# Kernel tuning notes

Hardware: AMD Instinct MI355X
Metric: run time of the kernel (lower is better)

## Reference

```python
import jax, jax.numpy as jnp
import numpy as np

SAMPLE_THRESH = 0.05  # self.sample_thresh


def grid_sample_bilinear_zeros(img, pts):
    """torch.nn.functional.grid_sample with mode='bilinear', align_corners=False,
    padding_mode='zeros'. img: [C, H, W]; pts: [N, 2] with (x, y) in [-1, 1].
    Returns [C, N]."""
    C, H, W = img.shape
    # align_corners=False unnormalization
    x = (pts[:, 0] + 1.0) * (W / 2.0) - 0.5
    y = (pts[:, 1] + 1.0) * (H / 2.0) - 0.5
    x0 = jnp.floor(x)
    y0 = jnp.floor(y)
    wx1 = x - x0
    wy1 = y - y0
    wx0 = 1.0 - wx1
    wy0 = 1.0 - wy1

    def gather(xi, yi):
        valid = (xi >= 0) & (xi < W) & (yi >= 0) & (yi < H)
        xi_c = jnp.clip(xi, 0, W - 1).astype(jnp.int32)
        yi_c = jnp.clip(yi, 0, H - 1).astype(jnp.int32)
        v = img[:, yi_c, xi_c]  # [C, N]
        return v * valid.astype(img.dtype)[None, :]

    out = (gather(x0, y0) * (wx0 * wy0)[None, :]
           + gather(x0 + 1, y0) * (wx1 * wy0)[None, :]
           + gather(x0, y0 + 1) * (wx0 * wy1)[None, :]
           + gather(x0 + 1, y0 + 1) * (wx1 * wy1)[None, :])
    return out


def setup_inputs() -> dict:
    key = jax.random.key(0)
    k1, k2, k3, k4 = jax.random.split(key, 4)
    N_A, N_B = 8192, 8192
    H, W2 = 504, 1008  # warp is [hs, 2*ws, 4] per post_process
    x_A = jax.random.uniform(k1, (N_A, 2), jnp.float32, -1.0, 1.0)
    x_B = jax.random.uniform(k2, (N_B, 2), jnp.float32, -1.0, 1.0)
    warp = jax.random.uniform(k3, (H, W2, 4), jnp.float32, -1.0, 1.0)
    certainty = jax.random.uniform(k4, (H, W2), jnp.float32, 0.0, 1.0)
    return {"x_A": x_A, "x_B": x_B, "warp": warp, "certainty": certainty}


def reference(x_A, x_B, warp, certainty):
    # --- match_keypoints ---
    # x_A_to_B = grid_sample(warp[..., -2:].permute(2,0,1)[None], x_A[None,None])[0,:,0].mT
    flow_img = jnp.transpose(warp[..., -2:], (2, 0, 1))  # [2, H, 2W]
    x_A_to_B = grid_sample_bilinear_zeros(flow_img, x_A).T  # [N_A, 2]
    cert_A_to_B = grid_sample_bilinear_zeros(certainty[None], x_A)[0]  # [N_A]

    # D = torch.cdist(x_A_to_B, x_B) via |a|^2 + |b|^2 - 2 a.b
    a2 = jnp.sum(x_A_to_B * x_A_to_B, axis=-1)  # [N_A]
    b2 = jnp.sum(x_B * x_B, axis=-1)            # [N_B]
    D2 = a2[:, None] + b2[None, :] - 2.0 * (x_A_to_B @ x_B.T)
    D = jnp.sqrt(jnp.maximum(D2, 1e-12))  # [N_A, N_B]

    # mutual nearest-neighbor mask with certainty threshold
    row_min = jnp.min(D, axis=-1, keepdims=True)
    col_min = jnp.min(D, axis=-2, keepdims=True)
    mask = (D == row_min) & (D == col_min) & (cert_A_to_B[:, None] > SAMPLE_THRESH)

    # jit-compatible equivalent of torch.nonzero: distances at mutual-NN pairs,
    # zero elsewhere. nonzero entries == matched (inds_A, inds_B) pairs.
    return jnp.where(mask, D, 0.0)
```

## Files before the change

kernel.cpp:

```cpp
#include <hip/hip_runtime.h>
#include <math.h>

#define SAMPLE_THRESH 0.05f

typedef float f32x4 __attribute__((ext_vector_type(4)));

__device__ __forceinline__ float d2_exact(float xa0, float xa1, float a2,
                                          float xb0, float xb1, float b2) {
    float p  = __fmul_rn(xa1, xb1);
    float q  = __fmaf_rn(xa0, xb0, p);
    float s  = __fadd_rn(a2, b2);
    return __fmaf_rn(-2.0f, q, s);
}

__device__ __forceinline__ float f_D(float d2) {
    return __fsqrt_rn(fmaxf(d2, 1e-12f));
}

__device__ __forceinline__ float nextf_pos(float x) {
    return __int_as_float(__float_as_int(x) + 1);
}
__device__ __forceinline__ float prevf_pos(float x) {
    return __int_as_float(__float_as_int(x) - 1);
}

__device__ __forceinline__ float hi_thresh(float m) {
    float t = f_D(m);
    float x = fmaxf(m, __fmul_rn(t, t));
    while (f_D(x) > t) x = prevf_pos(x);
    while (f_D(nextf_pos(x)) <= t) x = nextf_pos(x);
    return x;
}

__global__ __launch_bounds__(256) void sample_kernel(
    const float* __restrict__ xA, const float* __restrict__ xB,
    const float4* __restrict__ warp, const float* __restrict__ cert,
    float4* __restrict__ Apack, float4* __restrict__ Bpack,
    int nA, int nB, int H, int W) {
    int i = blockIdx.x * blockDim.x + threadIdx.x;
    if (i < nA) {
        float px = xA[2 * i + 0], py = xA[2 * i + 1];
        float xf = (px + 1.0f) * (0.5f * (float)W) - 0.5f;
        float yf = (py + 1.0f) * (0.5f * (float)H) - 0.5f;
        float x0f = floorf(xf), y0f = floorf(yf);
        float wx1 = xf - x0f, wy1 = yf - y0f;
        float wx0 = 1.0f - wx1, wy0 = 1.0f - wy1;
        int x0 = (int)x0f, y0 = (int)y0f;
        float fx = 0.0f, fy = 0.0f, cv = 0.0f;
#pragma unroll
        for (int dy = 0; dy < 2; ++dy) {
#pragma unroll
            for (int dx = 0; dx < 2; ++dx) {
                int xi = x0 + dx, yi = y0 + dy;
                float vm = (xi >= 0 && xi < W && yi >= 0 && yi < H) ? 1.0f : 0.0f;
                int xc = min(max(xi, 0), W - 1);
                int yc = min(max(yi, 0), H - 1);
                int idx = yc * W + xc;
                float4 wv = warp[idx];
                float  c  = cert[idx];
                float wgt = (dx ? wx1 : wx0) * (dy ? wy1 : wy0);
                fx += (wv.z * vm) * wgt;
                fy += (wv.w * vm) * wgt;
                cv += (c    * vm) * wgt;
            }
        }
        float a2 = fx * fx + fy * fy;
        Apack[i] = make_float4(fx, fy, a2, cv);
    }
    if (i < nB) {
        float b0 = xB[2 * i + 0], b1 = xB[2 * i + 1];
        Bpack[i] = make_float4(b0, b1, b0 * b0 + b1 * b1, 0.0f);
    }
}

__global__ __launch_bounds__(256) void min_kernel(
    const float4* __restrict__ Apack, const float4* __restrict__ Bpack,
    float4* __restrict__ rowpack, float* __restrict__ rowD,
    float4* __restrict__ colpack, int nA, int nB) {
    int gwave = (int)((blockIdx.x * blockDim.x + threadIdx.x) >> 6);
    int lane = threadIdx.x & 63;
    int nRowWaves = nA / 8;
    float m0 = 1e30f, m1 = 1e30f, m2 = 1e30f, m3 = 1e30f;
    float m4 = 1e30f, m5 = 1e30f, m6 = 1e30f, m7 = 1e30f;
    if (gwave < nRowWaves) {
        int i0 = gwave * 8;
        float4 A0 = Apack[i0 + 0], A1 = Apack[i0 + 1], A2 = Apack[i0 + 2], A3 = Apack[i0 + 3];
        float4 A4 = Apack[i0 + 4], A5 = Apack[i0 + 5], A6 = Apack[i0 + 6], A7 = Apack[i0 + 7];
        for (int j = lane; j < nB; j += 64) {
            float4 b = Bpack[j];
            m0 = fminf(m0, d2_exact(A0.x, A0.y, A0.z, b.x, b.y, b.z));
            m1 = fminf(m1, d2_exact(A1.x, A1.y, A1.z, b.x, b.y, b.z));
            m2 = fminf(m2, d2_exact(A2.x, A2.y, A2.z, b.x, b.y, b.z));
            m3 = fminf(m3, d2_exact(A3.x, A3.y, A3.z, b.x, b.y, b.z));
            m4 = fminf(m4, d2_exact(A4.x, A4.y, A4.z, b.x, b.y, b.z));
            m5 = fminf(m5, d2_exact(A5.x, A5.y, A5.z, b.x, b.y, b.z));
            m6 = fminf(m6, d2_exact(A6.x, A6.y, A6.z, b.x, b.y, b.z));
            m7 = fminf(m7, d2_exact(A7.x, A7.y, A7.z, b.x, b.y, b.z));
        }
#pragma unroll
        for (int o = 32; o; o >>= 1) {
            m0 = fminf(m0, __shfl_xor(m0, o, 64)); m1 = fminf(m1, __shfl_xor(m1, o, 64));
            m2 = fminf(m2, __shfl_xor(m2, o, 64)); m3 = fminf(m3, __shfl_xor(m3, o, 64));
            m4 = fminf(m4, __shfl_xor(m4, o, 64)); m5 = fminf(m5, __shfl_xor(m5, o, 64));
            m6 = fminf(m6, __shfl_xor(m6, o, 64)); m7 = fminf(m7, __shfl_xor(m7, o, 64));
        }
        if (lane == 0) {
#define ROW_OUT(K, AK, MK)                                                         \
            {                                                                      \
                float Dm = f_D(MK);                                                \
                float hi = (AK.w > SAMPLE_THRESH) ? hi_thresh(MK) : -1e30f;        \
                rowpack[i0 + K] = make_float4(AK.x, AK.y, AK.z, hi);               \
                rowD[i0 + K] = Dm;                                                 \
            }
            ROW_OUT(0, A0, m0) ROW_OUT(1, A1, m1) ROW_OUT(2, A2, m2) ROW_OUT(3, A3, m3)
            ROW_OUT(4, A4, m4) ROW_OUT(5, A5, m5) ROW_OUT(6, A6, m6) ROW_OUT(7, A7, m7)
#undef ROW_OUT
        }
    } else {
        int j0 = (gwave - nRowWaves) * 8;
        if (j0 >= nB) return;
        float4 B0 = Bpack[j0 + 0], B1 = Bpack[j0 + 1], B2 = Bpack[j0 + 2], B3 = Bpack[j0 + 3];
        float4 B4 = Bpack[j0 + 4], B5 = Bpack[j0 + 5], B6 = Bpack[j0 + 6], B7 = Bpack[j0 + 7];
        for (int i = lane; i < nA; i += 64) {
            float4 a = Apack[i];
            m0 = fminf(m0, d2_exact(a.x, a.y, a.z, B0.x, B0.y, B0.z));
            m1 = fminf(m1, d2_exact(a.x, a.y, a.z, B1.x, B1.y, B1.z));
            m2 = fminf(m2, d2_exact(a.x, a.y, a.z, B2.x, B2.y, B2.z));
            m3 = fminf(m3, d2_exact(a.x, a.y, a.z, B3.x, B3.y, B3.z));
            m4 = fminf(m4, d2_exact(a.x, a.y, a.z, B4.x, B4.y, B4.z));
            m5 = fminf(m5, d2_exact(a.x, a.y, a.z, B5.x, B5.y, B5.z));
            m6 = fminf(m6, d2_exact(a.x, a.y, a.z, B6.x, B6.y, B6.z));
            m7 = fminf(m7, d2_exact(a.x, a.y, a.z, B7.x, B7.y, B7.z));
        }
#pragma unroll
        for (int o = 32; o; o >>= 1) {
            m0 = fminf(m0, __shfl_xor(m0, o, 64)); m1 = fminf(m1, __shfl_xor(m1, o, 64));
            m2 = fminf(m2, __shfl_xor(m2, o, 64)); m3 = fminf(m3, __shfl_xor(m3, o, 64));
            m4 = fminf(m4, __shfl_xor(m4, o, 64)); m5 = fminf(m5, __shfl_xor(m5, o, 64));
            m6 = fminf(m6, __shfl_xor(m6, o, 64)); m7 = fminf(m7, __shfl_xor(m7, o, 64));
        }
        if (lane == 0) {
#define COL_OUT(K, BK, MK)                                                         \
            colpack[j0 + K] = make_float4(BK.x, BK.y, BK.z, hi_thresh(MK));
            COL_OUT(0, B0, m0) COL_OUT(1, B1, m1) COL_OUT(2, B2, m2) COL_OUT(3, B3, m3)
            COL_OUT(4, B4, m4) COL_OUT(5, B5, m5) COL_OUT(6, B6, m6) COL_OUT(7, B7, m7)
#undef COL_OUT
        }
    }
}

#define TI 64
#define TJ 1024
__global__ __launch_bounds__(256) void out_kernel(
    const float4* __restrict__ rowpack, const float* __restrict__ rowD,
    const float4* __restrict__ colpack, float* __restrict__ out, int N) {
    __shared__ float4 cp[TJ];
    __shared__ float4 rp[TI];
    __shared__ float rd[TI];
    int tid = threadIdx.x;
    int j0 = blockIdx.x * TJ;
    int i0 = blockIdx.y * TI;
    for (int k = tid; k < TJ; k += 256) cp[k] = colpack[j0 + k];
    if (tid < TI) { rp[tid] = rowpack[i0 + tid]; rd[tid] = rowD[i0 + tid]; }
    __syncthreads();
    float4 c0 = cp[tid * 4 + 0], c1 = cp[tid * 4 + 1];
    float4 c2 = cp[tid * 4 + 2], c3 = cp[tid * 4 + 3];
    size_t base = (size_t)i0 * (size_t)N + (size_t)j0 + (size_t)tid * 4;
#pragma unroll 2
    for (int r = 0; r < TI; ++r) {
        float4 a = rp[r];
        float Dm = rd[r];
        float d0 = d2_exact(a.x, a.y, a.z, c0.x, c0.y, c0.z);
        float d1 = d2_exact(a.x, a.y, a.z, c1.x, c1.y, c1.z);
        float d2 = d2_exact(a.x, a.y, a.z, c2.x, c2.y, c2.z);
        float d3 = d2_exact(a.x, a.y, a.z, c3.x, c3.y, c3.z);
        f32x4 o;
        o.x = (d0 <= a.w && d0 <= c0.w) ? Dm : 0.0f;
        o.y = (d1 <= a.w && d1 <= c1.w) ? Dm : 0.0f;
        o.z = (d2 <= a.w && d2 <= c2.w) ? Dm : 0.0f;
        o.w = (d3 <= a.w && d3 <= c3.w) ? Dm : 0.0f;
        __builtin_nontemporal_store(o, (f32x4*)(out + base + (size_t)r * (size_t)N));
    }
}

extern "C" void kernel_launch(void* const* d_in, const int* in_sizes, int n_in,
                              void* d_out, int out_size, void* d_ws, size_t ws_size,
                              hipStream_t stream) {
    const float* xA   = (const float*)d_in[0];
    const float* xB   = (const float*)d_in[1];
    const float* warp = (const float*)d_in[2];
    const float* cert = (const float*)d_in[3];
    int nA = in_sizes[0] / 2;
    int nB = in_sizes[1] / 2;
    const int H = 504, W = 1008;
    float* out = (float*)d_out;

    char* ws = (char*)d_ws;
    float4* Apack   = (float4*)ws;
    float4* Bpack   = Apack + nA;
    float4* rowpack = Bpack + nB;
    float4* colpack = rowpack + nA;
    float*  rowD    = (float*)(colpack + nB);

    int nmax = nA > nB ? nA : nB;
    sample_kernel<<<(nmax + 255) / 256, 256, 0, stream>>>(
        xA, xB, (const float4*)warp, cert, Apack, Bpack, nA, nB, H, W);

    int totWaves = nA / 8 + nB / 8;
    min_kernel<<<(totWaves * 64 + 255) / 256, 256, 0, stream>>>(
        Apack, Bpack, rowpack, rowD, colpack, nA, nB);

    dim3 grid(nB / TJ, nA / TI);
    out_kernel<<<grid, 256, 0, stream>>>(rowpack, rowD, colpack, out, nB);
}
```

Measured before the change: 330.8 us.

## Replace dense output kernel with zero-fill plus sparse scatter of matches

The fused compute-and-write output kernel is replaced by two steps: a grid-stride kernel that zero-fills the whole 8192x8192 output with nontemporal stores, and a scatter kernel in which each wave recomputes distances for 8 rows against all columns and writes only the mutual-nearest-neighbor entries. This separates the bandwidth-bound fill from the compare work, so the fill runs without any arithmetic. The cost is an extra full pass of comparisons, repeated colpack reads in the scatter kernel, and an additional kernel launch.

```diff
diff --git a/kernel.cpp b/kernel.cpp
--- a/kernel.cpp
+++ b/kernel.cpp
@@ -149,37 +149,36 @@
     }
 }
 
-#define TI 64
-#define TJ 1024
-__global__ __launch_bounds__(256) void out_kernel(
+__global__ __launch_bounds__(256) void fill_kernel(f32x4* __restrict__ out, long long n4) {
+    long long stride = (long long)gridDim.x * 256;
+    f32x4 z = {0.0f, 0.0f, 0.0f, 0.0f};
+    for (long long k = (long long)blockIdx.x * 256 + threadIdx.x; k < n4; k += stride)
+        __builtin_nontemporal_store(z, out + k);
+}
+
+__global__ __launch_bounds__(256) void scatter_kernel(
     const float4* __restrict__ rowpack, const float* __restrict__ rowD,
-    const float4* __restrict__ colpack, float* __restrict__ out, int N) {
-    __shared__ float4 cp[TJ];
-    __shared__ float4 rp[TI];
-    __shared__ float rd[TI];
-    int tid = threadIdx.x;
-    int j0 = blockIdx.x * TJ;
-    int i0 = blockIdx.y * TI;
-    for (int k = tid; k < TJ; k += 256) cp[k] = colpack[j0 + k];
-    if (tid < TI) { rp[tid] = rowpack[i0 + tid]; rd[tid] = rowD[i0 + tid]; }
-    __syncthreads();
-    float4 c0 = cp[tid * 4 + 0], c1 = cp[tid * 4 + 1];
-    float4 c2 = cp[tid * 4 + 2], c3 = cp[tid * 4 + 3];
-    size_t base = (size_t)i0 * (size_t)N + (size_t)j0 + (size_t)tid * 4;
-#pragma unroll 2
-    for (int r = 0; r < TI; ++r) {
-        float4 a = rp[r];
-        float Dm = rd[r];
-        float d0 = d2_exact(a.x, a.y, a.z, c0.x, c0.y, c0.z);
-        float d1 = d2_exact(a.x, a.y, a.z, c1.x, c1.y, c1.z);
-        float d2 = d2_exact(a.x, a.y, a.z, c2.x, c2.y, c2.z);
-        float d3 = d2_exact(a.x, a.y, a.z, c3.x, c3.y, c3.z);
-        f32x4 o;
-        o.x = (d0 <= a.w && d0 <= c0.w) ? Dm : 0.0f;
-        o.y = (d1 <= a.w && d1 <= c1.w) ? Dm : 0.0f;
-        o.z = (d2 <= a.w && d2 <= c2.w) ? Dm : 0.0f;
-        o.w = (d3 <= a.w && d3 <= c3.w) ? Dm : 0.0f;
-        __builtin_nontemporal_store(o, (f32x4*)(out + base + (size_t)r * (size_t)N));
+    const float4* __restrict__ colpack, float* __restrict__ out,
+    int nA, int nB) {
+    int wave = (int)((blockIdx.x * blockDim.x + threadIdx.x) >> 6);
+    int lane = threadIdx.x & 63;
+    int i0 = wave * 8;
+    if (i0 >= nA) return;
+    float4 A0 = rowpack[i0 + 0], A1 = rowpack[i0 + 1], A2 = rowpack[i0 + 2], A3 = rowpack[i0 + 3];
+    float4 A4 = rowpack[i0 + 4], A5 = rowpack[i0 + 5], A6 = rowpack[i0 + 6], A7 = rowpack[i0 + 7];
+    float D0 = rowD[i0 + 0], D1 = rowD[i0 + 1], D2v = rowD[i0 + 2], D3 = rowD[i0 + 3];
+    float D4 = rowD[i0 + 4], D5 = rowD[i0 + 5], D6 = rowD[i0 + 6], D7 = rowD[i0 + 7];
+    for (int j = lane; j < nB; j += 64) {
+        float4 c = colpack[j];
+#define ROW_TEST(K, AK, DK)                                                        \
+        {                                                                          \
+            float d2 = d2_exact(AK.x, AK.y, AK.z, c.x, c.y, c.z);                  \
+            if (d2 <= AK.w && d2 <= c.w)                                           \
+                out[(size_t)(i0 + K) * (size_t)nB + (size_t)j] = DK;               \
+        }
+        ROW_TEST(0, A0, D0) ROW_TEST(1, A1, D1) ROW_TEST(2, A2, D2v) ROW_TEST(3, A3, D3)
+        ROW_TEST(4, A4, D4) ROW_TEST(5, A5, D5) ROW_TEST(6, A6, D6) ROW_TEST(7, A7, D7)
+#undef ROW_TEST
     }
 }
 
@@ -202,6 +201,9 @@
     float4* colpack = rowpack + nA;
     float*  rowD    = (float*)(colpack + nB);
 
+    long long n4 = (long long)out_size / 4;
+    fill_kernel<<<8192, 256, 0, stream>>>((f32x4*)out, n4);
+
     int nmax = nA > nB ? nA : nB;
     sample_kernel<<<(nmax + 255) / 256, 256, 0, stream>>>(
         xA, xB, (const float4*)warp, cert, Apack, Bpack, nA, nB, H, W);
@@ -210,6 +212,7 @@
     min_kernel<<<(totWaves * 64 + 255) / 256, 256, 0, stream>>>(
         Apack, Bpack, rowpack, rowD, colpack, nA, nB);
 
-    dim3 grid(nB / TJ, nA / TI);
-    out_kernel<<<grid, 256, 0, stream>>>(rowpack, rowD, colpack, out, nB);
-}
+    int rowWaves = nA / 8;
+    scatter_kernel<<<(rowWaves * 64 + 255) / 256, 256, 0, stream>>>(
+        rowpack, rowD, colpack, out, nA, nB);
+}
```

New measurement: 406.2 us. 22.8% more time.
